# Kernel tuning notes

Hardware: AMD Instinct MI355X
Metric: run time of the kernel (lower is better)

Reference implementation:

```python
import jax, jax.numpy as jnp
import numpy as np

B, C, N = 32, 512, 1024   # batch, input channels, tokens
E, D, H = 512, 2048, 8    # d_input, d_model, heads
T, O = 50, 1000           # iterations, out_dims
NA, NO = 512, 512         # n_synch_action, n_synch_out


def setup_inputs() -> dict:
    key = jax.random.key(0)
    ks = jax.random.split(key, 16)
    s = 0.02
    rn = lambda k, shape: jax.random.normal(k, shape, jnp.float32) * s
    return dict(
        x=jax.random.normal(ks[0], (B, C, N), jnp.float32),
        W_kv=rn(ks[1], (C, E)), b_kv=jnp.zeros(E), g_kv=jnp.ones(E), be_kv=jnp.zeros(E),
        W_q=rn(ks[2], (NA, E)), b_q=jnp.zeros(E),
        W_in=rn(ks[3], (E, 3 * E)), b_in=jnp.zeros(3 * E),
        W_ao=rn(ks[4], (E, E)), b_ao=jnp.zeros(E),
        W_syn=rn(ks[5], (E + D, 2 * D)), b_syn=jnp.zeros(2 * D),
        g_syn=jnp.ones(D), be_syn=jnp.zeros(D),
        g_pm=jnp.ones(D), be_pm=jnp.zeros(D),
        W1=rn(ks[6], (D, D)), b1=jnp.zeros(D),
        W2=rn(ks[7], (D, D)), b2=jnp.zeros(D),
        start_state=jax.random.uniform(ks[8], (D,), jnp.float32, -0.1, 0.1),
        decay_action=jnp.zeros(NA), decay_out=jnp.zeros(NO),
        W_out=rn(ks[9], (NO, O)), b_out=jnp.zeros(O),
        idx_action=jax.random.permutation(ks[10], D)[:NA].astype(jnp.int32),
        idx_out=jax.random.permutation(ks[11], D)[:NO].astype(jnp.int32),
    )


def _ln(x, g, b, eps=1e-5):
    m = x.mean(-1, keepdims=True)
    v = ((x - m) ** 2).mean(-1, keepdims=True)
    return (x - m) * jax.lax.rsqrt(v + eps) * g + b


def reference(x, W_kv, b_kv, g_kv, be_kv, W_q, b_q, W_in, b_in, W_ao, b_ao,
              W_syn, b_syn, g_syn, be_syn, g_pm, be_pm, W1, b1, W2, b2,
              start_state, decay_action, decay_out, W_out, b_out,
              idx_action, idx_out):
    Bx = x.shape[0]
    hd = E // H
    # features: backbone='none', pos='none' -> flatten(2).transpose(1,2) then kv_proj
    feats = jnp.transpose(x, (0, 2, 1))                 # [B,N,C]
    kv = _ln(feats @ W_kv + b_kv, g_kv, be_kv)          # [B,N,E]
    # MHA K/V are constant across iterations -> hoist
    Wq_a, Wk_a, Wv_a = jnp.split(W_in, 3, axis=1)
    bq_a, bk_a, bv_a = jnp.split(b_in, 3)
    K = (kv @ Wk_a + bk_a).reshape(Bx, N, H, hd)
    V = (kv @ Wv_a + bv_a).reshape(Bx, N, H, hd)
    r_a = jnp.exp(-jnp.clip(decay_action, 0.0, 15.0))   # [NA]
    r_o = jnp.exp(-jnp.clip(decay_out, 0.0, 15.0))      # [NO]
    act0 = jnp.broadcast_to(start_state, (Bx, D))
    zA = jnp.zeros((Bx, NA), jnp.float32)
    zO = jnp.zeros((Bx, NO), jnp.float32)
    logO = jnp.log(jnp.float32(O))
    scale = 1.0 / jnp.sqrt(jnp.float32(hd))

    def step(carry, _):
        act, aA, bA, aO, bO = carry
        # action sync (left == right in the source, so products are squares)
        sel = act[:, idx_action]
        aA = r_a * aA + sel * sel
        bA = r_a * bA + 1.0
        syncA = aA * jax.lax.rsqrt(bA)                  # [B,NA]
        # cross-attention query
        q = syncA @ W_q + b_q                           # [B,E]
        qh = (q @ Wq_a + bq_a).reshape(Bx, H, hd)
        scores = jnp.einsum('bhd,bnhd->bhn', qh, K) * scale
        w = jax.nn.softmax(scores, axis=-1)
        attn = jnp.einsum('bhn,bnhd->bhd', w, V).reshape(Bx, E)
        attn = attn @ W_ao + b_ao
        # synapses: LazyLinear(2D) -> GLU -> LayerNorm (dropout=0)
        h = jnp.concatenate([attn, act], axis=-1) @ W_syn + b_syn
        a_half, g_half = jnp.split(h, 2, axis=-1)
        state = _ln(a_half * jax.nn.sigmoid(g_half), g_syn, be_syn)
        # post-synapse MLP: LN -> Linear -> ReLU -> Linear -> ReLU
        hpm = _ln(state, g_pm, be_pm)
        act = jax.nn.relu(jax.nn.relu(hpm @ W1 + b1) @ W2 + b2)
        # out sync
        selo = act[:, idx_out]
        aO = r_o * aO + selo * selo
        bO = r_o * bO + 1.0
        syncO = aO * jax.lax.rsqrt(bO)                  # [B,NO]
        pred = syncO @ W_out + b_out                    # [B,O]
        lp = jax.nn.log_softmax(pred, axis=-1)
        ne = -jnp.sum(jnp.exp(lp) * lp, axis=-1) / logO
        cert = jnp.stack([ne, 1.0 - ne], axis=-1)       # [B,2]
        return (act, aA, bA, aO, bO), (pred, cert, syncO)

    _, (preds, certs, syncs) = jax.lax.scan(step, (act0, zA, zA, zO, zO), None, length=T)
    predictions = jnp.transpose(preds, (1, 2, 0))       # [B,O,T]
    certainties = jnp.transpose(certs, (1, 2, 0))       # [B,2,T]
    return predictions, certainties, syncs[-1]
```

## Files before the change

kernel.cpp:

```cpp
#include <hip/hip_runtime.h>


typedef unsigned short u16;
typedef unsigned int uv4 __attribute__((ext_vector_type(4)));
typedef float fv4 __attribute__((ext_vector_type(4)));
typedef float fv2 __attribute__((ext_vector_type(2)));

__device__ __forceinline__ float bf2f(u16 u) {
    return __uint_as_float(((unsigned int)u) << 16);
}
__device__ __forceinline__ float bflo(unsigned int u) { return __uint_as_float(u << 16); }
__device__ __forceinline__ float bfhi(unsigned int u) { return __uint_as_float(u & 0xffff0000u); }
__device__ __forceinline__ u16 f2bf(float f) {
    unsigned int u = __float_as_uint(f);
    unsigned int r = u + 0x7fffu + ((u >> 16) & 1u);
    return (u16)(r >> 16);
}

__device__ __forceinline__ void cload(fv4& r, const void* p) {
    asm volatile("global_load_dwordx4 %0, %1, off sc0 sc1" : "=v"(r) : "v"(p));
}
__device__ __forceinline__ void cload2(fv2& r, const void* p) {
    asm volatile("global_load_dwordx2 %0, %1, off sc0 sc1" : "=v"(r) : "v"(p));
}
__device__ __forceinline__ void cstore4(void* p, fv4 v) {
    asm volatile("global_store_dwordx4 %0, %1, off sc0 sc1" :: "v"(p), "v"(v) : "memory");
}
__device__ __forceinline__ void cstore2(void* p, fv2 v) {
    asm volatile("global_store_dwordx2 %0, %1, off sc0 sc1" :: "v"(p), "v"(v) : "memory");
}
__device__ __forceinline__ void cwait1(fv4& a) {
    asm volatile("s_waitcnt vmcnt(0)" : "+v"(a) :: "memory");
    __builtin_amdgcn_sched_barrier(0);
}
__device__ __forceinline__ void cwait2(fv4& a, fv4& b) {
    asm volatile("s_waitcnt vmcnt(0)" : "+v"(a), "+v"(b) :: "memory");
    __builtin_amdgcn_sched_barrier(0);
}
__device__ __forceinline__ void cwait4(fv4& a, fv4& b, fv4& c, fv4& d) {
    asm volatile("s_waitcnt vmcnt(0)" : "+v"(a), "+v"(b), "+v"(c), "+v"(d) :: "memory");
    __builtin_amdgcn_sched_barrier(0);
}
__device__ __forceinline__ void cwait2x4(fv2& a, fv2& b, fv2& c, fv2& d) {
    asm volatile("s_waitcnt vmcnt(0)" : "+v"(a), "+v"(b), "+v"(c), "+v"(d) :: "memory");
    __builtin_amdgcn_sched_barrier(0);
}

__device__ __forceinline__ float aload(const float* p) {
    return __hip_atomic_load((const float*)p, __ATOMIC_RELAXED, __HIP_MEMORY_SCOPE_AGENT);
}

__global__ __launch_bounds__(256) void k_init(
    const float* __restrict__ start_state, const float* __restrict__ dec_a,
    const float* __restrict__ dec_o,
    float* act0, float* aA, float* bA, float* aO, float* bO,
    float* r_a, float* r_o, unsigned* bar)
{
    int g = blockIdx.x * 256 + threadIdx.x;
    int T = gridDim.x * 256;
    for (int i = g; i < 32 * 2048; i += T) act0[i] = start_state[i & 2047];
    for (int i = g; i < 32 * 512; i += T) { aA[i] = 0.f; bA[i] = 0.f; aO[i] = 0.f; bO[i] = 0.f; }
    for (int i = g; i < 512; i += T) {
        float da = fminf(fmaxf(dec_a[i], 0.f), 15.f);
        float dv = fminf(fmaxf(dec_o[i], 0.f), 15.f);
        r_a[i] = __expf(-da);
        r_o[i] = __expf(-dv);
    }
    if (g < 2048) bar[g] = 0u;
}

__global__ __launch_bounds__(256) void k_gemm_xT(
    const float* __restrict__ x, const float* __restrict__ Wkv,
    const float* __restrict__ bkv, float* __restrict__ out)
{
    __shared__ float As[16 * 68];
    __shared__ float Bs[16 * 132];
    int tid = threadIdx.x;
    int tn = tid & 15, tm = tid >> 4;
    int n0 = blockIdx.x * 128;
    int r0 = blockIdx.y * 64;
    int b = r0 >> 10;
    int nrow0 = r0 & 1023;
    const float* xb = x + (size_t)b * 512 * 1024;
    float acc[4][8];
#pragma unroll
    for (int i = 0; i < 4; ++i)
#pragma unroll
        for (int j = 0; j < 8; ++j) acc[i][j] = 0.f;

    for (int k0 = 0; k0 < 512; k0 += 16) {
        __syncthreads();
#pragma unroll
        for (int l = 0; l < 4; ++l) {
            int i = tid + l * 256;
            int nn = i & 63, kk = i >> 6;
            As[kk * 68 + nn] = xb[(size_t)(k0 + kk) * 1024 + nrow0 + nn];
        }
#pragma unroll
        for (int l = 0; l < 8; ++l) {
            int i = tid + l * 256;
            int n = i & 127, kk = i >> 7;
            Bs[kk * 132 + n] = Wkv[(size_t)(k0 + kk) * 512 + n0 + n];
        }
        __syncthreads();
#pragma unroll
        for (int k = 0; k < 16; ++k) {
            float4 a4 = *(const float4*)&As[k * 68 + tm * 4];
            float4 b0 = *(const float4*)&Bs[k * 132 + tn * 8];
            float4 b1 = *(const float4*)&Bs[k * 132 + tn * 8 + 4];
            float av[4] = {a4.x, a4.y, a4.z, a4.w};
            float bv[8] = {b0.x, b0.y, b0.z, b0.w, b1.x, b1.y, b1.z, b1.w};
#pragma unroll
            for (int i = 0; i < 4; ++i)
#pragma unroll
                for (int j = 0; j < 8; ++j) acc[i][j] += av[i] * bv[j];
        }
    }
#pragma unroll
    for (int i = 0; i < 4; ++i) {
        int r = r0 + tm * 4 + i;
        int c = n0 + tn * 8;
        float* orow = out + (size_t)r * 512 + c;
#pragma unroll
        for (int j = 0; j < 8; ++j) orow[j] = acc[i][j] + bkv[c + j];
    }
}

// ... 69 lines not shown
    float4 u1 = *(float4*)(p + 4);
    float v[8] = {u0.x, u0.y, u0.z, u0.w, u1.x, u1.y, u1.z, u1.w};
    float s = 0.f, s2 = 0.f;
#pragma unroll
    for (int i = 0; i < 8; ++i) { s += v[i]; s2 += v[i] * v[i]; }
#pragma unroll
    for (int off = 32; off >= 1; off >>= 1) {
        s += __shfl_xor(s, off, 64);
        s2 += __shfl_xor(s2, off, 64);
    }
    float m = s * (1.f / 512.f);
    float var = s2 * (1.f / 512.f) - m * m;
    float rs = rsqrtf(var + 1e-5f);
    const float* gp = g + lane * 8;
    const float* bp = be + lane * 8;
#pragma unroll
    for (int i = 0; i < 8; ++i) v[i] = (v[i] - m) * rs * gp[i] + bp[i];
    *(float4*)p = make_float4(v[0], v[1], v[2], v[3]);
    *(float4*)(p + 4) = make_float4(v[4], v[5], v[6], v[7]);
}

__global__ __launch_bounds__(256) void k_bvec(
    const float* __restrict__ vin, const float* __restrict__ B, int ldb,
    const float* __restrict__ badd, float* __restrict__ out, int Nj)
{
    int j = blockIdx.x * 256 + threadIdx.x;
    if (j >= Nj) return;
    float s = 0.f;
    for (int e = 0; e < 512; ++e) s += vin[e] * B[(size_t)e * ldb + j];
    out[j] = s + badd[j];
}

__global__ __launch_bounds__(256) void k_convert(
    const float* __restrict__ src, u16* __restrict__ dst, int n)
{
    int g = blockIdx.x * 256 + threadIdx.x;
    int T = gridDim.x * 256;
    for (int i = g; i < n; i += T) dst[i] = f2bf(src[i]);
}

__global__ __launch_bounds__(256) void k_transpose_wout(
    const float* __restrict__ W, u16* __restrict__ WT)
{
    int j = blockIdx.x * 256 + threadIdx.x;
    if (j >= 1000) return;
    for (int k = 0; k < 512; ++k) WT[(size_t)j * 512 + k] = f2bf(W[(size_t)k * 1000 + j]);
}

__global__ __launch_bounds__(256) void k_transpose_v(
    const u16* __restrict__ V, u16* __restrict__ VT)
{
    int bh = blockIdx.x;
    int b = bh >> 3, h = bh & 7;
    int tid = threadIdx.x;
    const u16* src = V + (size_t)b * 1024 * 512 + h * 64;
    u16* dst = VT + (size_t)bh * 64 * 1024;
    int n0 = tid * 4;
    for (int d = 0; d < 64; ++d) {
        u16 a0 = src[(size_t)(n0 + 0) * 512 + d];
        u16 a1 = src[(size_t)(n0 + 1) * 512 + d];
        u16 a2 = src[(size_t)(n0 + 2) * 512 + d];
        u16 a3 = src[(size_t)(n0 + 3) * 512 + d];
        uint2 w = make_uint2((unsigned)a0 | ((unsigned)a1 << 16),
                             (unsigned)a2 | ((unsigned)a3 << 16));
        *(uint2*)&dst[(size_t)d * 1024 + n0] = w;
    }
}

#define NBLK 1024

struct LoopP {
    const u16* Wqq; const float* bqq;
    const u16* K;   const u16* VT;
    const u16* Wfull; const float* bcomb;
    const u16* W1; const float* b1;
    const u16* W2; const float* b2;
    const u16* WoutT; const float* bout;
    const int* idxA; const int* idxO;
    const float* r_a; const float* r_o;
    float* aA0; float* aA1; float* bA0; float* bA1;
    float* aO0; float* aO1; float* bO0; float* bO1;
    float* act0; float* act1;
    float* pvp; float* mz;
    float* h_pre; float* hpm; float* t1;
    float* out;
    const float* gsyn; const float* besyn; const float* gpm; const float* bepm;
    unsigned* bar;
};

union Smem {
    struct { float sA[512]; float qh[64]; float sc[256]; float red[512]; } at;
    struct { float Al[32 * 36]; float wc[1024]; } sk;
    struct { float red[16]; } gl;
    struct { float sO[512]; float red[8]; } pr;
};

__device__ __forceinline__ void gridbar(unsigned* bar)
{
    __syncthreads();
    if (threadIdx.x == 0) {
        int blk = blockIdx.x;
        unsigned* cnt1 = bar + ((blk >> 6) << 5);
        unsigned* cnt2 = bar + (16 << 5);
        unsigned* genp = bar + ((17 + (blk & 31)) << 5);
        unsigned g = __hip_atomic_load(genp, __ATOMIC_RELAXED, __HIP_MEMORY_SCOPE_AGENT);
        asm volatile("s_waitcnt vmcnt(0)" ::: "memory");
        unsigned a = __hip_atomic_fetch_add(cnt1, 1u, __ATOMIC_RELAXED, __HIP_MEMORY_SCOPE_AGENT);
        if (a == 63u) {
            __hip_atomic_store(cnt1, 0u, __ATOMIC_RELAXED, __HIP_MEMORY_SCOPE_AGENT);
            asm volatile("s_waitcnt vmcnt(0)" ::: "memory");
            unsigned a2 = __hip_atomic_fetch_add(cnt2, 1u, __ATOMIC_RELAXED, __HIP_MEMORY_SCOPE_AGENT);
            if (a2 == 15u) {
                __hip_atomic_store(cnt2, 0u, __ATOMIC_RELAXED, __HIP_MEMORY_SCOPE_AGENT);
                asm volatile("s_waitcnt vmcnt(0)" ::: "memory");
#pragma unroll
                for (int r = 0; r < 32; ++r)
                    __hip_atomic_store(bar + ((17 + r) << 5), g + 1u,
                                       __ATOMIC_RELAXED, __HIP_MEMORY_SCOPE_AGENT);
            }
        }
        unsigned cur;
        do {
            cur = __hip_atomic_load(genp, __ATOMIC_RELAXED, __HIP_MEMORY_SCOPE_AGENT);
            if (cur != g) break;
            __builtin_amdgcn_s_sleep(2);
        } while (true);
        asm volatile("" ::: "memory");
    }
    __syncthreads();
}

__device__ __forceinline__ void red2(float& a, float& b, float* red, int tid)
{
#pragma unroll
    for (int off = 32; off >= 1; off >>= 1) {
        a += __shfl_xor(a, off, 64);
        b += __shfl_xor(b, off, 64);
    }
    __syncthreads();
    if ((tid & 63) == 0) { red[(tid >> 6) * 2] = a; red[(tid >> 6) * 2 + 1] = b; }
    __syncthreads();
    float sa = 0.f, sb = 0.f;
#pragma unroll
    for (int w = 0; w < 8; ++w) { sa += red[2 * w]; sb += red[2 * w + 1]; }
    a = sa; b = sb;
}

__global__ __launch_bounds__(512, 8) void k_loop(LoopP P)
{
    __shared__ Smem s;
    const int tid = threadIdx.x;
    const int blk = blockIdx.x;
    const int lane = tid & 63;
    const int wav = tid >> 6;

    for (int t = 0; t < 50; ++t) {
        const float* actprev = (t & 1) ? P.act1 : P.act0;
        float*       actnext = (t & 1) ? P.act0 : P.act1;
        const float* aAp = (t & 1) ? P.aA1 : P.aA0;  float* aAc = (t & 1) ? P.aA0 : P.aA1;
        const float* bAp = (t & 1) ? P.bA1 : P.bA0;  float* bAc = (t & 1) ? P.bA0 : P.bA1;
        const float* aOp = (t & 1) ? P.aO1 : P.aO0;  float* aOc = (t & 1) ? P.aO0 : P.aO1;
        const float* bOp = (t & 1) ? P.bO1 : P.bO0;  float* bOc = (t & 1) ? P.bO0 : P.bO1;

        __syncthreads();

        {
            int bh = blk >> 2, p = blk & 3;
            int b = bh >> 3, h = bh & 7;
            if (tid < 64) {
                int g4 = blk * 64 + tid;
                fv4 zz = {0.f, 0.f, 0.f, 0.f};
                if (g4 < 32768) cstore4(&P.h_pre[g4 * 4], zz);
                else if (g4 < 49152) cstore4(&P.t1[(g4 - 32768) * 4], zz);
                else cstore4(&actnext[(g4 - 49152) * 4], zz);
            }
            {
                int j = tid;
                int ia = P.idxA[j];
                float v = aload(&actprev[b * 2048 + ia]);
                if (t > 0) v = fmaxf(0.f, v + P.b2[ia]);
                float r = P.r_a[j];
                float a = r * aAp[b * 512 + j] + v * v;
                float bb = r * bAp[b * 512 + j] + 1.f;
                aAc[b * 512 + j] = a; bAc[b * 512 + j] = bb;
                s.at.sA[j] = a * rsqrtf(bb);
            }
            __syncthreads();
            {
                int d = tid & 63, kg = tid >> 6;
                const u16* wp = P.Wqq + (size_t)(kg * 64) * 512 + h * 64 + d;
                const float* ap = s.at.sA + kg * 64;
                float pq = 0.f;
#pragma unroll 16
                for (int k = 0; k < 64; ++k) pq += ap[k] * bf2f(wp[(size_t)k * 512]);
                s.at.red[tid] = pq;
            }
            __syncthreads();
            if (tid < 64) {
                float q = P.bqq[h * 64 + tid];
#pragma unroll
                for (int g2 = 0; g2 < 8; ++g2) q += s.at.red[g2 * 64 + tid];
                s.at.qh[tid] = q;
            }
            __syncthreads();
            if (tid < 256) {
                const u16* Kbh = P.K + (size_t)b * 1024 * 512 + h * 64;
                const uv4* kp = (const uv4*)(Kbh + (size_t)(p * 256 + tid) * 512);
                uv4 u[8];
#pragma unroll
                for (int i = 0; i < 8; ++i) u[i] = __builtin_nontemporal_load(kp + i);
                float dot = 0.f;
#pragma unroll
                for (int i = 0; i < 8; ++i) {
                    float4 q0 = *(float4*)&s.at.qh[i * 8];
                    float4 q1 = *(float4*)&s.at.qh[i * 8 + 4];
                    dot += q0.x * bflo(u[i].x) + q0.y * bfhi(u[i].x)
                         + q0.z * bflo(u[i].y) + q0.w * bfhi(u[i].y)
                         + q1.x * bflo(u[i].z) + q1.y * bfhi(u[i].z)
                         + q1.z * bflo(u[i].w) + q1.w * bfhi(u[i].w);
                }
                s.at.sc[tid] = dot * 0.125f;
            }
            __syncthreads();
            float mv = (tid < 256) ? s.at.sc[tid] : -1e30f;
#pragma unroll
            for (int off = 32; off >= 1; off >>= 1) mv = fmaxf(mv, __shfl_xor(mv, off, 64));
            if (lane == 0) s.at.red[wav] = mv;
            __syncthreads();
            float mloc = s.at.red[0];
#pragma unroll
            for (int w = 1; w < 8; ++w) mloc = fmaxf(mloc, s.at.red[w]);
            float ev = 0.f;
            if (tid < 256) {
                ev = __expf(s.at.sc[tid] - mloc);
                s.at.sc[tid] = ev;
            }
            float zv = ev;
#pragma unroll
            for (int off = 32; off >= 1; off >>= 1) zv += __shfl_xor(zv, off, 64);
            __syncthreads();
            if (lane == 0) s.at.red[wav] = zv;
            __syncthreads();
            float Zloc = 0.f;
#pragma unroll
            for (int w = 0; w < 8; ++w) Zloc += s.at.red[w];
            __syncthreads();
            {
                int d = tid & 63, ng = tid >> 6;
                const uv4* vp = (const uv4*)(P.VT
                    + ((size_t)bh * 64 + d) * 1024 + p * 256 + ng * 32);
                float acc = 0.f;
#pragma unroll
                for (int i = 0; i < 4; ++i) {
                    uv4 u = __builtin_nontemporal_load(vp + i);
                    const float* so = s.at.sc + ng * 32 + i * 8;
                    acc += so[0] * bflo(u.x) + so[1] * bfhi(u.x)
                         + so[2] * bflo(u.y) + so[3] * bfhi(u.y)
                         + so[4] * bflo(u.z) + so[5] * bfhi(u.z)
                         + so[6] * bflo(u.w) + so[7] * bfhi(u.w);
                }
                s.at.red[tid] = acc;
            }
            __syncthreads();
            if (tid < 64) {
                float a = 0.f;
#pragma unroll
                for (int g2 = 0; g2 < 8; ++g2) a += s.at.red[g2 * 64 + tid];
                s.at.qh[tid] = a;
            }
            __syncthreads();
            if (tid < 16) {
                fv4 v = *(fv4*)&s.at.qh[tid * 4];
                cstore4(&P.pvp[((size_t)p * 256 + bh) * 64 + tid * 4], v);
            }
            if (tid == 0) {
                fv2 v; v.x = mloc; v.y = Zloc;
                cstore2(&P.mz[(p * 256 + bh) * 2], v);
            }
        }
        gridbar(P.bar);

        {
            if (tid < 256) {
                int rh = tid;
                fv2 m0, m1, m2, m3;
                cload2(m0, &P.mz[(0 * 256 + rh) * 2]);
                cload2(m1, &P.mz[(1 * 256 + rh) * 2]);
                cload2(m2, &P.mz[(2 * 256 + rh) * 2]);
                cload2(m3, &P.mz[(3 * 256 + rh) * 2]);
                cwait2x4(m0, m1, m2, m3);
                float M = fmaxf(fmaxf(m0.x, m1.x), fmaxf(m2.x, m3.x));
                float e0 = __expf(m0.x - M), e1 = __expf(m1.x - M);
                float e2 = __expf(m2.x - M), e3 = __expf(m3.x - M);
                float Z = m0.y * e0 + m1.y * e1 + m2.y * e2 + m3.y * e3;
                float inv = 1.f / Z;
                s.sk.wc[rh * 4 + 0] = e0 * inv;
                s.sk.wc[rh * 4 + 1] = e1 * inv;
                s.sk.wc[rh * 4 + 2] = e2 * inv;
                s.sk.wc[rh * 4 + 3] = e3 * inv;
            }
            int kb = blk >> 6, jb = blk & 63;
            int j = jb * 64 + (tid & 63);
            int rg = tid >> 6;
            int kbeg = kb * 160;
            float a0 = 0.f, a1 = 0.f, a2 = 0.f, a3 = 0.f;
            for (int k0 = kbeg; k0 < kbeg + 160; k0 += 32) {
                __syncthreads();
                if (tid < 256) {
                    int k4 = (tid & 7) * 4, r = tid >> 3;
                    int kk = k0 + k4;
                    fv4 v;
                    if (kk < 512) {
                        int h = kk >> 6, d = kk & 63;
                        int rh = r * 8 + h;
                        fv4 v0, v1, v2, v3;
                        cload(v0, &P.pvp[((size_t)0 * 256 + rh) * 64 + d]);
                        cload(v1, &P.pvp[((size_t)1 * 256 + rh) * 64 + d]);
                        cload(v2, &P.pvp[((size_t)2 * 256 + rh) * 64 + d]);
                        cload(v3, &P.pvp[((size_t)3 * 256 + rh) * 64 + d]);
                        cwait4(v0, v1, v2, v3);
                        const float* w = &s.sk.wc[rh * 4];
                        v = v0 * w[0] + v1 * w[1] + v2 * w[2] + v3 * w[3];
                    } else {
                        cload(v, &actprev[r * 2048 + kk - 512]);
                        cwait1(v);
                        if (t > 0) {
                            float4 b4 = *(const float4*)&P.b2[kk - 512];
                            v.x = fmaxf(0.f, v.x + b4.x);
                            v.y = fmaxf(0.f, v.y + b4.y);
                            v.z = fmaxf(0.f, v.z + b4.z);
                            v.w = fmaxf(0.f, v.w + b4.w);
                        }
                    }
                    s.sk.Al[(k4 + 0) * 36 + r] = v.x;
                    s.sk.Al[(k4 + 1) * 36 + r] = v.y;
                    s.sk.Al[(k4 + 2) * 36 + r] = v.z;
                    s.sk.Al[(k4 + 3) * 36 + r] = v.w;
                }
                __syncthreads();
                const u16* wp = P.Wfull + (size_t)k0 * 4096 + j;
#pragma unroll 32
                for (int k = 0; k < 32; ++k) {
                    float w = bf2f(wp[(size_t)k * 4096]);
                    float4 a = *(const float4*)&s.sk.Al[k * 36 + rg * 4];
                    a0 += a.x * w; a1 += a.y * w; a2 += a.z * w; a3 += a.w * w;
                }
            }
            int r0 = rg * 4;
            atomicAdd(&P.h_pre[(size_t)(r0 + 0) * 4096 + j], a0);
            atomicAdd(&P.h_pre[(size_t)(r0 + 1) * 4096 + j], a1);
            atomicAdd(&P.h_pre[(size_t)(r0 + 2) * 4096 + j], a2);
            atomicAdd(&P.h_pre[(size_t)(r0 + 3) * 4096 + j], a3);
        }
        gridbar(P.bar);

        if (blk < 32) {
            const float* hr = P.h_pre + (size_t)blk * 4096;
            int i4 = tid * 4;
            fv4 av, gv;
            cload(av, hr + i4);
            cload(gv, hr + 2048 + i4);
            cwait2(av, gv);
            float4 bc1 = *(const float4*)&P.bcomb[i4];
            float4 bc2 = *(const float4*)&P.bcomb[2048 + i4];
            fv4 z;
            z.x = (av.x + bc1.x) / (1.f + __expf(-(gv.x + bc2.x)));
            z.y = (av.y + bc1.y) / (1.f + __expf(-(gv.y + bc2.y)));
            z.z = (av.z + bc1.z) / (1.f + __expf(-(gv.z + bc2.z)));
            z.w = (av.w + bc1.w) / (1.f + __expf(-(gv.w + bc2.w)));
            float sa = z.x + z.y + z.z + z.w;
            float sb = z.x * z.x + z.y * z.y + z.z * z.z + z.w * z.w;
            red2(sa, sb, s.gl.red, tid);
            float m1 = sa * (1.f / 2048.f);
            float v1 = sb * (1.f / 2048.f) - m1 * m1;
            float rs1 = rsqrtf(v1 + 1e-5f);
            float4 gs = *(const float4*)&P.gsyn[i4];
            float4 bs = *(const float4*)&P.besyn[i4];
            z.x = (z.x - m1) * rs1 * gs.x + bs.x;
            z.y = (z.y - m1) * rs1 * gs.y + bs.y;
            z.z = (z.z - m1) * rs1 * gs.z + bs.z;
            z.w = (z.w - m1) * rs1 * gs.w + bs.w;
            float ta = z.x + z.y + z.z + z.w;
            float tb = z.x * z.x + z.y * z.y + z.z * z.z + z.w * z.w;
            red2(ta, tb, s.gl.red, tid);
            float m2 = ta * (1.f / 2048.f);
            float v2 = tb * (1.f / 2048.f) - m2 * m2;
            float rs2 = rsqrtf(v2 + 1e-5f);
            float4 gp = *(const float4*)&P.gpm[i4];
            float4 bp = *(const float4*)&P.bepm[i4];
            fv4 o;
            o.x = (z.x - m2) * rs2 * gp.x + bp.x;
            o.y = (z.y - m2) * rs2 * gp.y + bp.y;
            o.z = (z.z - m2) * rs2 * gp.z + bp.z;
            o.w = (z.w - m2) * rs2 * gp.w + bp.w;
            cstore4(&P.hpm[(size_t)blk * 2048 + i4], o);
        }
        gridbar(P.bar);

        {
            int kb = blk >> 5, jb = blk & 31;
            int j = jb * 64 + (tid & 63);
            int rg = tid >> 6;
            int kbeg = kb * 64;
            float a0 = 0.f, a1 = 0.f, a2 = 0.f, a3 = 0.f;
            for (int k0 = kbeg; k0 < kbeg + 64; k0 += 32) {
                __syncthreads();
                if (tid < 256) {
                    int k4 = (tid & 7) * 4, r = tid >> 3;
                    fv4 v;
                    cload(v, &P.hpm[r * 2048 + k0 + k4]);
                    cwait1(v);
                    s.sk.Al[(k4 + 0) * 36 + r] = v.x;
                    s.sk.Al[(k4 + 1) * 36 + r] = v.y;
                    s.sk.Al[(k4 + 2) * 36 + r] = v.z;
                    s.sk.Al[(k4 + 3) * 36 + r] = v.w;
                }
                __syncthreads();
                const u16* wp = P.W1 + (size_t)k0 * 2048 + j;
#pragma unroll 32
                for (int k = 0; k < 32; ++k) {
                    float w = bf2f(wp[(size_t)k * 2048]);
                    float4 a = *(const float4*)&s.sk.Al[k * 36 + rg * 4];
                    a0 += a.x * w; a1 += a.y * w; a2 += a.z * w; a3 += a.w * w;
                }
            }
            int r0 = rg * 4;
            atomicAdd(&P.t1[(r0 + 0) * 2048 + j], a0);
            atomicAdd(&P.t1[(r0 + 1) * 2048 + j], a1);
            atomicAdd(&P.t1[(r0 + 2) * 2048 + j], a2);
            atomicAdd(&P.t1[(r0 + 3) * 2048 + j], a3);
        }
        gridbar(P.bar);

        {
            int kb = blk >> 5, jb = blk & 31;
            int j = jb * 64 + (tid & 63);
            int rg = tid >> 6;
            int kbeg = kb * 64;
            float a0 = 0.f, a1 = 0.f, a2 = 0.f, a3 = 0.f;
            for (int k0 = kbeg; k0 < kbeg + 64; k0 += 32) {
                __syncthreads();
                if (tid < 256) {
                    int k4 = (tid & 7) * 4, r = tid >> 3;
                    int kk = k0 + k4;
                    fv4 v;
                    cload(v, &P.t1[r * 2048 + kk]);
                    cwait1(v);
                    float4 b4 = *(const float4*)&P.b1[kk];
                    s.sk.Al[(k4 + 0) * 36 + r] = fmaxf(0.f, v.x + b4.x);
                    s.sk.Al[(k4 + 1) * 36 + r] = fmaxf(0.f, v.y + b4.y);
                    s.sk.Al[(k4 + 2) * 36 + r] = fmaxf(0.f, v.z + b4.z);
                    s.sk.Al[(k4 + 3) * 36 + r] = fmaxf(0.f, v.w + b4.w);
                }
                __syncthreads();
                const u16* wp = P.W2 + (size_t)k0 * 2048 + j;
#pragma unroll 32
                for (int k = 0; k < 32; ++k) {
                    float w = bf2f(wp[(size_t)k * 2048]);
                    float4 a = *(const float4*)&s.sk.Al[k * 36 + rg * 4];
                    a0 += a.x * w; a1 += a.y * w; a2 += a.z * w; a3 += a.w * w;
                }
            }
            int r0 = rg * 4;
            atomicAdd(&actnext[(r0 + 0) * 2048 + j], a0);
            atomicAdd(&actnext[(r0 + 1) * 2048 + j], a1);
            atomicAdd(&actnext[(r0 + 2) * 2048 + j], a2);
            atomicAdd(&actnext[(r0 + 3) * 2048 + j], a3);
        }
        gridbar(P.bar);

        if (blk < 32) {
            int b = blk;
            {
                int j2 = tid;
                int io = P.idxO[j2];
                float v = fmaxf(0.f, aload(&actnext[b * 2048 + io]) + P.b2[io]);
                float r = P.r_o[j2];
                float a = r * aOp[b * 512 + j2] + v * v;
                float bb = r * bOp[b * 512 + j2] + 1.f;
                aOc[b * 512 + j2] = a; bOc[b * 512 + j2] = bb;
                float sy = a * rsqrtf(bb);
                s.pr.sO[j2] = sy;
                if (t == 49) P.out[1603200 + b * 512 + j2] = sy;
            }
            __syncthreads();
            bool has1 = tid < 488;
            float p0, p1 = -1e30f;
            {
                const uint4* wp = (const uint4*)(P.WoutT + (size_t)tid * 512);
                float acc = 0.f;
#pragma unroll 16
                for (int i = 0; i < 64; ++i) {
                    uint4 u = wp[i];
                    const float* so = s.pr.sO + i * 8;
                    acc += so[0] * bflo(u.x) + so[1] * bfhi(u.x)
                         + so[2] * bflo(u.y) + so[3] * bfhi(u.y)
                         + so[4] * bflo(u.z) + so[5] * bfhi(u.z)
                         + so[6] * bflo(u.w) + so[7] * bfhi(u.w);
                }
                p0 = acc + P.bout[tid];
            }
            if (has1) {
                const uint4* wp = (const uint4*)(P.WoutT + (size_t)(tid + 512) * 512);
                float acc = 0.f;
#pragma unroll 16
                for (int i = 0; i < 64; ++i) {
                    uint4 u = wp[i];
                    const float* so = s.pr.sO + i * 8;
                    acc += so[0] * bflo(u.x) + so[1] * bfhi(u.x)
                         + so[2] * bflo(u.y) + so[3] * bfhi(u.y)
                         + so[4] * bflo(u.z) + so[5] * bfhi(u.z)
                         + so[6] * bflo(u.w) + so[7] * bfhi(u.w);
                }
                p1 = acc + P.bout[tid + 512];
            }
            float mx = fmaxf(p0, p1);
#pragma unroll
            for (int off = 32; off >= 1; off >>= 1) mx = fmaxf(mx, __shfl_xor(mx, off, 64));
            __syncthreads();
            if (lane == 0) s.pr.red[wav] = mx;
            __syncthreads();
            mx = s.pr.red[0];
#pragma unroll
            for (int w = 1; w < 8; ++w) mx = fmaxf(mx, s.pr.red[w]);
            float zs = __expf(p0 - mx) + (has1 ? __expf(p1 - mx) : 0.f);
#pragma unroll
            for (int off = 32; off >= 1; off >>= 1) zs += __shfl_xor(zs, off, 64);
            __syncthreads();
            if (lane == 0) s.pr.red[wav] = zs;
            __syncthreads();
            float Z = 0.f;
#pragma unroll
            for (int w = 0; w < 8; ++w) Z += s.pr.red[w];
            float logZ = __logf(Z);
            float lp0 = p0 - mx - logZ;
            float se = __expf(lp0) * lp0;
            if (has1) { float lp1 = p1 - mx - logZ; se += __expf(lp1) * lp1; }
#pragma unroll
            for (int off = 32; off >= 1; off >>= 1) se += __shfl_xor(se, off, 64);
            __syncthreads();
            if (lane == 0) s.pr.red[wav] = se;
            __syncthreads();
            float S = 0.f;
#pragma unroll
            for (int w = 0; w < 8; ++w) S += s.pr.red[w];
            float ne = -S / logf(1000.0f);
            P.out[(size_t)b * 50000 + (size_t)tid * 50 + t] = p0;
            if (has1) P.out[(size_t)b * 50000 + (size_t)(tid + 512) * 50 + t] = p1;
            if (tid == 0) {
                P.out[1600000 + b * 100 + t] = ne;
                P.out[1600000 + b * 100 + 50 + t] = 1.f - ne;
            }
        }
    }
}

extern "C" void kernel_launch(void* const* d_in, const int* in_sizes, int n_in,
                              void* d_out, int out_size, void* d_ws, size_t ws_size,
                              hipStream_t stream)
{
    const float* x      = (const float*)d_in[0];
    const float* W_kv   = (const float*)d_in[1];
    const float* b_kv   = (const float*)d_in[2];
    const float* g_kv   = (const float*)d_in[3];
    const float* be_kv  = (const float*)d_in[4];
    const float* W_q    = (const float*)d_in[5];
    const float* b_q    = (const float*)d_in[6];
    const float* W_in   = (const float*)d_in[7];
    const float* b_in   = (const float*)d_in[8];
    const float* W_ao   = (const float*)d_in[9];
    const float* b_ao   = (const float*)d_in[10];
    const float* W_syn  = (const float*)d_in[11];
    const float* b_syn  = (const float*)d_in[12];
    const float* g_syn  = (const float*)d_in[13];
    const float* be_syn = (const float*)d_in[14];
    const float* g_pm   = (const float*)d_in[15];
    const float* be_pm  = (const float*)d_in[16];
    const float* W1     = (const float*)d_in[17];
    const float* b1     = (const float*)d_in[18];
    const float* W2     = (const float*)d_in[19];
    const float* b2     = (const float*)d_in[20];
    const float* start_state  = (const float*)d_in[21];
    const float* decay_action = (const float*)d_in[22];
    const float* decay_out    = (const float*)d_in[23];
    const float* W_out  = (const float*)d_in[24];
    const float* b_out  = (const float*)d_in[25];
    const int* idx_action = (const int*)d_in[26];
    const int* idx_out    = (const int*)d_in[27];
    float* out = (float*)d_out;

    char* ws = (char*)d_ws;
    size_t off = 0;
    auto take = [&](size_t bytes) -> char* {
        char* p = ws + off;
        off += (bytes + 255) & ~(size_t)255;
        return p;
    };

    char* region0 = take(67108864);
    float* kv = (float*)region0;
    u16* W_full = (u16*)region0;
    u16* W1b    = (u16*)(region0 + 20971520);
    u16* W2b    = (u16*)(region0 + 29360128);
    u16* WoutT  = (u16*)(region0 + 37748736);
    u16* Wqqb   = (u16*)(region0 + 38772736);

    u16* K_bf = (u16*)take(33554432);
    u16* V_bf = (u16*)take(33554432);
    u16* V_T  = (u16*)take(33554432);
    float* b_qq   = (float*)take(2048);
    float* b_comb = (float*)take(16384);
    float* r_a = (float*)take(2048);
    float* r_o = (float*)take(2048);
    float* aA0 = (float*)take(65536);
    float* aA1 = (float*)take(65536);
    float* bA0 = (float*)take(65536);
    float* bA1 = (float*)take(65536);
    float* aO0 = (float*)take(65536);
    float* aO1 = (float*)take(65536);
    float* bO0 = (float*)take(65536);
    float* bO1 = (float*)take(65536);
    float* act0v = (float*)take(262144);
    float* act1v = (float*)take(262144);
    float* h_pre = (float*)take(524288);
    float* hpm   = (float*)take(262144);
    float* t1_pre = (float*)take(262144);
    float* pvp = (float*)take(262144);
    float* mzB = (float*)take(8192);
    unsigned* bar = (unsigned*)take(8192);
    (void)ws_size; (void)in_sizes; (void)n_in; (void)out_size;

    k_init<<<256, 256, 0, stream>>>(start_state, decay_action, decay_out,
                                    act0v, aA0, bA0, aO0, bO0, r_a, r_o, bar);
    k_gemm_xT<<<dim3(4, 512), 256, 0, stream>>>(x, W_kv, b_kv, kv);
    k_ln_kv<<<8192, 256, 0, stream>>>(kv, g_kv, be_kv);
    k_gemm_AB<<<dim3(4, 512), 256, 0, stream>>>(kv, 512, W_in + 512, 1536, b_in + 512, K_bf, 512);
    k_gemm_AB<<<dim3(4, 512), 256, 0, stream>>>(kv, 512, W_in + 1024, 1536, b_in + 1024, V_bf, 512);
    k_transpose_v<<<256, 256, 0, stream>>>(V_bf, V_T);
    k_gemm_AB<<<dim3(4, 8), 256, 0, stream>>>(W_q, 512, W_in, 1536, nullptr, Wqqb, 512);
    k_gemm_AB<<<dim3(32, 8), 256, 0, stream>>>(W_ao, 512, W_syn, 4096, nullptr, W_full, 4096);
    k_bvec<<<2, 256, 0, stream>>>(b_q, W_in, 1536, b_in, b_qq, 512);
    k_bvec<<<16, 256, 0, stream>>>(b_ao, W_syn, 4096, b_syn, b_comb, 4096);
    k_convert<<<2048, 256, 0, stream>>>(W_syn + (size_t)512 * 4096, W_full + (size_t)512 * 4096, 2048 * 4096);
    k_convert<<<2048, 256, 0, stream>>>(W1, W1b, 2048 * 2048);
    k_convert<<<2048, 256, 0, stream>>>(W2, W2b, 2048 * 2048);
    k_transpose_wout<<<4, 256, 0, stream>>>(W_out, WoutT);

    LoopP p;
    p.Wqq = Wqqb; p.bqq = b_qq;
    p.K = K_bf;   p.VT = V_T;
    p.Wfull = W_full; p.bcomb = b_comb;
    p.W1 = W1b; p.b1 = b1;
    p.W2 = W2b; p.b2 = b2;
    p.WoutT = WoutT; p.bout = b_out;
    p.idxA = idx_action; p.idxO = idx_out;
    p.r_a = r_a; p.r_o = r_o;
    p.aA0 = aA0; p.aA1 = aA1; p.bA0 = bA0; p.bA1 = bA1;
    p.aO0 = aO0; p.aO1 = aO1; p.bO0 = bO0; p.bO1 = bO1;
    p.act0 = act0v; p.act1 = act1v;
    p.pvp = pvp; p.mz = mzB;
    p.h_pre = h_pre; p.hpm = hpm; p.t1 = t1_pre;
    p.out = out;
    p.gsyn = g_syn; p.besyn = be_syn; p.gpm = g_pm; p.bepm = be_pm;
    p.bar = bar;

    k_loop<<<dim3(NBLK), dim3(512), 0, stream>>>(p);
}
```

Before: 10.34 ms.

## Partition persistent-loop GEMVs by batch row instead of split-K with atomics

Reworks the three per-iteration matrix products (synapse, W1, W2) so each block owns one batch row and a column chunk, reducing over K inside the block through shared memory and writing results with plain stores. This removes the atomicAdd accumulation and the per-iteration zeroing of h_pre, t1 and act. The softmax-combined attention row and the relu'd previous activation are now precomputed into new buffers, which costs an extra grid barrier and phase. In exchange each block rereads its weight columns once per batch row, so total weight traffic from L2 rises by the batch factor compared with the old row-tiled reuse.

```diff
diff --git a/kernel.cpp b/kernel.cpp
--- a/kernel.cpp
+++ b/kernel.cpp
@@ -37,12 +37,8 @@
     asm volatile("s_waitcnt vmcnt(0)" : "+v"(a), "+v"(b) :: "memory");
     __builtin_amdgcn_sched_barrier(0);
 }
-__device__ __forceinline__ void cwait4(fv4& a, fv4& b, fv4& c, fv4& d) {
-    asm volatile("s_waitcnt vmcnt(0)" : "+v"(a), "+v"(b), "+v"(c), "+v"(d) :: "memory");
-    __builtin_amdgcn_sched_barrier(0);
-}
-__device__ __forceinline__ void cwait2x4(fv2& a, fv2& b, fv2& c, fv2& d) {
-    asm volatile("s_waitcnt vmcnt(0)" : "+v"(a), "+v"(b), "+v"(c), "+v"(d) :: "memory");
+__device__ __forceinline__ void cwaitf2(fv2& a) {
+    asm volatile("s_waitcnt vmcnt(0)" : "+v"(a) :: "memory");
     __builtin_amdgcn_sched_barrier(0);
 }
 
@@ -278,6 +274,7 @@
     float* aO0; float* aO1; float* bO0; float* bO1;
     float* act0; float* act1;
     float* pvp; float* mz;
+    float* attn_f; float* actR;
     float* h_pre; float* hpm; float* t1;
     float* out;
     const float* gsyn; const float* besyn; const float* gpm; const float* bepm;
@@ -286,7 +283,9 @@
 
 union Smem {
     struct { float sA[512]; float qh[64]; float sc[256]; float red[512]; } at;
-    struct { float Al[32 * 36]; float wc[1024]; } sk;
+    struct { float mzs[64]; float arow[512]; } b2;
+    struct { float As[2560]; float red[512]; float orow[128]; } ck;
+    struct { float As[2048]; float red[512]; float orow[64]; } ek;
     struct { float red[16]; } gl;
     struct { float sO[512]; float red[8]; } pr;
 };
@@ -363,12 +362,19 @@
         {
             int bh = blk >> 2, p = blk & 3;
             int b = bh >> 3, h = bh & 7;
-            if (tid < 64) {
-                int g4 = blk * 64 + tid;
-                fv4 zz = {0.f, 0.f, 0.f, 0.f};
-                if (g4 < 32768) cstore4(&P.h_pre[g4 * 4], zz);
-                else if (g4 < 49152) cstore4(&P.t1[(g4 - 32768) * 4], zz);
-                else cstore4(&actnext[(g4 - 49152) * 4], zz);
+            if (p == 0 && tid < 64) {
+                int i4 = (h * 64 + tid) * 4;
+                fv4 v;
+                cload(v, &actprev[b * 2048 + i4]);
+                cwait1(v);
+                if (t > 0) {
+                    float4 b4 = *(const float4*)&P.b2[i4];
+                    v.x = fmaxf(0.f, v.x + b4.x);
+                    v.y = fmaxf(0.f, v.y + b4.y);
+                    v.z = fmaxf(0.f, v.z + b4.z);
+                    v.w = fmaxf(0.f, v.w + b4.w);
+                }
+                cstore4(&P.actR[b * 2048 + i4], v);
             }
             {
                 int j = tid;
@@ -476,77 +482,73 @@
         }
         gridbar(P.bar);
 
+        if (blk < 32) {
+            int b = blk;
+            if (tid < 32) {
+                int p = tid >> 3, h = tid & 7;
+                fv2 v;
+                cload2(v, &P.mz[(p * 256 + b * 8 + h) * 2]);
+                cwaitf2(v);
+                s.b2.mzs[tid * 2] = v.x;
+                s.b2.mzs[tid * 2 + 1] = v.y;
+            }
+            __syncthreads();
+            int h = tid >> 6, d = tid & 63;
+            int rh = b * 8 + h;
+            float m0 = s.b2.mzs[(0 * 8 + h) * 2], z0 = s.b2.mzs[(0 * 8 + h) * 2 + 1];
+            float m1 = s.b2.mzs[(1 * 8 + h) * 2], z1 = s.b2.mzs[(1 * 8 + h) * 2 + 1];
+            float m2 = s.b2.mzs[(2 * 8 + h) * 2], z2 = s.b2.mzs[(2 * 8 + h) * 2 + 1];
+            float m3 = s.b2.mzs[(3 * 8 + h) * 2], z3 = s.b2.mzs[(3 * 8 + h) * 2 + 1];
+            float M = fmaxf(fmaxf(m0, m1), fmaxf(m2, m3));
+            float e0 = __expf(m0 - M), e1 = __expf(m1 - M);
+            float e2 = __expf(m2 - M), e3 = __expf(m3 - M);
+            float Zinv = 1.f / (z0 * e0 + z1 * e1 + z2 * e2 + z3 * e3);
+            float acc = aload(&P.pvp[((size_t)0 * 256 + rh) * 64 + d]) * e0
+                      + aload(&P.pvp[((size_t)1 * 256 + rh) * 64 + d]) * e1
+                      + aload(&P.pvp[((size_t)2 * 256 + rh) * 64 + d]) * e2
+                      + aload(&P.pvp[((size_t)3 * 256 + rh) * 64 + d]) * e3;
+            s.b2.arow[tid] = acc * Zinv;
+            __syncthreads();
+            if (tid < 128) {
+                fv4 v = *(fv4*)&s.b2.arow[tid * 4];
+                cstore4(&P.attn_f[b * 512 + tid * 4], v);
+            }
+        }
+        gridbar(P.bar);
+
         {
-            if (tid < 256) {
-                int rh = tid;
-                fv2 m0, m1, m2, m3;
-                cload2(m0, &P.mz[(0 * 256 + rh) * 2]);
-                cload2(m1, &P.mz[(1 * 256 + rh) * 2]);
-                cload2(m2, &P.mz[(2 * 256 + rh) * 2]);
-                cload2(m3, &P.mz[(3 * 256 + rh) * 2]);
-                cwait2x4(m0, m1, m2, m3);
-                float M = fmaxf(fmaxf(m0.x, m1.x), fmaxf(m2.x, m3.x));
-                float e0 = __expf(m0.x - M), e1 = __expf(m1.x - M);
-                float e2 = __expf(m2.x - M), e3 = __expf(m3.x - M);
-                float Z = m0.y * e0 + m1.y * e1 + m2.y * e2 + m3.y * e3;
-                float inv = 1.f / Z;
-                s.sk.wc[rh * 4 + 0] = e0 * inv;
-                s.sk.wc[rh * 4 + 1] = e1 * inv;
-                s.sk.wc[rh * 4 + 2] = e2 * inv;
-                s.sk.wc[rh * 4 + 3] = e3 * inv;
-            }
-            int kb = blk >> 6, jb = blk & 63;
-            int j = jb * 64 + (tid & 63);
-            int rg = tid >> 6;
-            int kbeg = kb * 160;
-            float a0 = 0.f, a1 = 0.f, a2 = 0.f, a3 = 0.f;
-            for (int k0 = kbeg; k0 < kbeg + 160; k0 += 32) {
-                __syncthreads();
-                if (tid < 256) {
-                    int k4 = (tid & 7) * 4, r = tid >> 3;
-                    int kk = k0 + k4;
-                    fv4 v;
-                    if (kk < 512) {
-                        int h = kk >> 6, d = kk & 63;
-                        int rh = r * 8 + h;
-                        fv4 v0, v1, v2, v3;
-                        cload(v0, &P.pvp[((size_t)0 * 256 + rh) * 64 + d]);
-                        cload(v1, &P.pvp[((size_t)1 * 256 + rh) * 64 + d]);
-                        cload(v2, &P.pvp[((size_t)2 * 256 + rh) * 64 + d]);
-                        cload(v3, &P.pvp[((size_t)3 * 256 + rh) * 64 + d]);
-                        cwait4(v0, v1, v2, v3);
-                        const float* w = &s.sk.wc[rh * 4];
-                        v = v0 * w[0] + v1 * w[1] + v2 * w[2] + v3 * w[3];
-                    } else {
-                        cload(v, &actprev[r * 2048 + kk - 512]);
-                        cwait1(v);
-                        if (t > 0) {
-                            float4 b4 = *(const float4*)&P.b2[kk - 512];
-                            v.x = fmaxf(0.f, v.x + b4.x);
-                            v.y = fmaxf(0.f, v.y + b4.y);
-                            v.z = fmaxf(0.f, v.z + b4.z);
-                            v.w = fmaxf(0.f, v.w + b4.w);
-                        }
-                    }
-                    s.sk.Al[(k4 + 0) * 36 + r] = v.x;
-                    s.sk.Al[(k4 + 1) * 36 + r] = v.y;
-                    s.sk.Al[(k4 + 2) * 36 + r] = v.z;
-                    s.sk.Al[(k4 + 3) * 36 + r] = v.w;
-                }
-                __syncthreads();
-                const u16* wp = P.Wfull + (size_t)k0 * 4096 + j;
+            int b = blk >> 5, jc = blk & 31;
+            int j0 = jc * 128;
+            if (tid < 128) {
+                fv4 v; cload(v, &P.attn_f[b * 512 + tid * 4]); cwait1(v);
+                *(fv4*)&s.ck.As[tid * 4] = v;
+            } else {
+                fv4 v; cload(v, &P.actR[b * 2048 + (tid - 128) * 4]); cwait1(v);
+                *(fv4*)&s.ck.As[512 + (tid - 128) * 4] = v;
+            }
+            if (tid < 128) {
+                fv4 v; cload(v, &P.actR[b * 2048 + (384 + tid) * 4]); cwait1(v);
+                *(fv4*)&s.ck.As[512 + (384 + tid) * 4] = v;
+            }
+            __syncthreads();
+            int j = j0 + (tid & 127);
+            int kq = tid >> 7;
+            const u16* wp = P.Wfull + (size_t)(kq * 640) * 4096 + j;
+            const float* ap = s.ck.As + kq * 640;
+            float acc = 0.f;
 #pragma unroll 32
-                for (int k = 0; k < 32; ++k) {
-                    float w = bf2f(wp[(size_t)k * 4096]);
-                    float4 a = *(const float4*)&s.sk.Al[k * 36 + rg * 4];
-                    a0 += a.x * w; a1 += a.y * w; a2 += a.z * w; a3 += a.w * w;
-                }
-            }
-            int r0 = rg * 4;
-            atomicAdd(&P.h_pre[(size_t)(r0 + 0) * 4096 + j], a0);
-            atomicAdd(&P.h_pre[(size_t)(r0 + 1) * 4096 + j], a1);
-            atomicAdd(&P.h_pre[(size_t)(r0 + 2) * 4096 + j], a2);
-            atomicAdd(&P.h_pre[(size_t)(r0 + 3) * 4096 + j], a3);
+            for (int k = 0; k < 640; ++k) acc += ap[k] * bf2f(wp[(size_t)k * 4096]);
+            s.ck.red[kq * 128 + (tid & 127)] = acc;
+            __syncthreads();
+            if (tid < 128) {
+                s.ck.orow[tid] = s.ck.red[tid] + s.ck.red[128 + tid]
+                               + s.ck.red[256 + tid] + s.ck.red[384 + tid];
+            }
+            __syncthreads();
+            if (tid < 32) {
+                fv4 v = *(fv4*)&s.ck.orow[tid * 4];
+                cstore4(&P.h_pre[(size_t)b * 4096 + j0 + tid * 4], v);
+            }
         }
         gridbar(P.bar);
 
@@ -594,74 +596,67 @@
         gridbar(P.bar);
 
         {
-            int kb = blk >> 5, jb = blk & 31;
-            int j = jb * 64 + (tid & 63);
-            int rg = tid >> 6;
-            int kbeg = kb * 64;
-            float a0 = 0.f, a1 = 0.f, a2 = 0.f, a3 = 0.f;
-            for (int k0 = kbeg; k0 < kbeg + 64; k0 += 32) {
-                __syncthreads();
-                if (tid < 256) {
-                    int k4 = (tid & 7) * 4, r = tid >> 3;
-                    fv4 v;
-                    cload(v, &P.hpm[r * 2048 + k0 + k4]);
-                    cwait1(v);
-                    s.sk.Al[(k4 + 0) * 36 + r] = v.x;
-                    s.sk.Al[(k4 + 1) * 36 + r] = v.y;
-                    s.sk.Al[(k4 + 2) * 36 + r] = v.z;
-                    s.sk.Al[(k4 + 3) * 36 + r] = v.w;
-                }
-                __syncthreads();
-                const u16* wp = P.W1 + (size_t)k0 * 2048 + j;
+            int b = blk >> 5, jc = blk & 31;
+            int j0 = jc * 64;
+            {
+                fv4 v; cload(v, &P.hpm[(size_t)b * 2048 + tid * 4]); cwait1(v);
+                *(fv4*)&s.ek.As[tid * 4] = v;
+            }
+            __syncthreads();
+            int j = j0 + (tid & 63), kq = tid >> 6;
+            const u16* wp = P.W1 + (size_t)(kq * 256) * 2048 + j;
+            const float* ap = s.ek.As + kq * 256;
+            float acc = 0.f;
 #pragma unroll 32
-                for (int k = 0; k < 32; ++k) {
-                    float w = bf2f(wp[(size_t)k * 2048]);
-                    float4 a = *(const float4*)&s.sk.Al[k * 36 + rg * 4];
-                    a0 += a.x * w; a1 += a.y * w; a2 += a.z * w; a3 += a.w * w;
-                }
-            }
-            int r0 = rg * 4;
-            atomicAdd(&P.t1[(r0 + 0) * 2048 + j], a0);
-            atomicAdd(&P.t1[(r0 + 1) * 2048 + j], a1);
-            atomicAdd(&P.t1[(r0 + 2) * 2048 + j], a2);
-            atomicAdd(&P.t1[(r0 + 3) * 2048 + j], a3);
+            for (int k = 0; k < 256; ++k) acc += ap[k] * bf2f(wp[(size_t)k * 2048]);
+            s.ek.red[kq * 64 + (tid & 63)] = acc;
+            __syncthreads();
+            if (tid < 64) {
+                float v = 0.f;
+#pragma unroll
+                for (int q = 0; q < 8; ++q) v += s.ek.red[q * 64 + tid];
+                s.ek.orow[tid] = v;
+            }
+            __syncthreads();
+            if (tid < 16) {
+                fv4 v = *(fv4*)&s.ek.orow[tid * 4];
+                cstore4(&P.t1[(size_t)b * 2048 + j0 + tid * 4], v);
+            }
         }
         gridbar(P.bar);
 
         {
-            int kb = blk >> 5, jb = blk & 31;
-            int j = jb * 64 + (tid & 63);
-            int rg = tid >> 6;
-            int kbeg = kb * 64;
-            float a0 = 0.f, a1 = 0.f, a2 = 0.f, a3 = 0.f;
-            for (int k0 = kbeg; k0 < kbeg + 64; k0 += 32) {
-                __syncthreads();
-                if (tid < 256) {
-                    int k4 = (tid & 7) * 4, r = tid >> 3;
-                    int kk = k0 + k4;
-                    fv4 v;
-                    cload(v, &P.t1[r * 2048 + kk]);
-                    cwait1(v);
-                    float4 b4 = *(const float4*)&P.b1[kk];
-                    s.sk.Al[(k4 + 0) * 36 + r] = fmaxf(0.f, v.x + b4.x);
-                    s.sk.Al[(k4 + 1) * 36 + r] = fmaxf(0.f, v.y + b4.y);
-                    s.sk.Al[(k4 + 2) * 36 + r] = fmaxf(0.f, v.z + b4.z);
-                    s.sk.Al[(k4 + 3) * 36 + r] = fmaxf(0.f, v.w + b4.w);
-                }
-                __syncthreads();
-                const u16* wp = P.W2 + (size_t)k0 * 2048 + j;
+            int b = blk >> 5, jc = blk & 31;
+            int j0 = jc * 64;
+            {
+                fv4 v; cload(v, &P.t1[(size_t)b * 2048 + tid * 4]); cwait1(v);
+                float4 b4 = *(const float4*)&P.b1[tid * 4];
+                v.x = fmaxf(0.f, v.x + b4.x);
+                v.y = fmaxf(0.f, v.y + b4.y);
+                v.z = fmaxf(0.f, v.z + b4.z);
+                v.w = fmaxf(0.f, v.w + b4.w);
+                *(fv4*)&s.ek.As[tid * 4] = v;
+            }
+            __syncthreads();
+            int j = j0 + (tid & 63), kq = tid >> 6;
+            const u16* wp = P.W2 + (size_t)(kq * 256) * 2048 + j;
+            const float* ap = s.ek.As + kq * 256;
+            float acc = 0.f;
 #pragma unroll 32
-                for (int k = 0; k < 32; ++k) {
-                    float w = bf2f(wp[(size_t)k * 2048]);
-                    float4 a = *(const float4*)&s.sk.Al[k * 36 + rg * 4];
-                    a0 += a.x * w; a1 += a.y * w; a2 += a.z * w; a3 += a.w * w;
-                }
-            }
-            int r0 = rg * 4;
-            atomicAdd(&actnext[(r0 + 0) * 2048 + j], a0);
-            atomicAdd(&actnext[(r0 + 1) * 2048 + j], a1);
-            atomicAdd(&actnext[(r0 + 2) * 2048 + j], a2);
-            atomicAdd(&actnext[(r0 + 3) * 2048 + j], a3);
+            for (int k = 0; k < 256; ++k) acc += ap[k] * bf2f(wp[(size_t)k * 2048]);
+            s.ek.red[kq * 64 + (tid & 63)] = acc;
+            __syncthreads();
+            if (tid < 64) {
+                float v = 0.f;
+#pragma unroll
+                for (int q = 0; q < 8; ++q) v += s.ek.red[q * 64 + tid];
+                s.ek.orow[tid] = v;
+            }
+            __syncthreads();
+            if (tid < 16) {
+                fv4 v = *(fv4*)&s.ek.orow[tid * 4];
+                cstore4(&actnext[(size_t)b * 2048 + j0 + tid * 4], v);
+            }
         }
         gridbar(P.bar);
 
@@ -823,6 +818,8 @@
     float* t1_pre = (float*)take(262144);
     float* pvp = (float*)take(262144);
     float* mzB = (float*)take(8192);
+    float* attn_f = (float*)take(65536);
+    float* actR   = (float*)take(262144);
     unsigned* bar = (unsigned*)take(8192);
     (void)ws_size; (void)in_sizes; (void)n_in; (void)out_size;
 
@@ -855,6 +852,7 @@
     p.aO0 = aO0; p.aO1 = aO1; p.bO0 = bO0; p.bO1 = bO1;
     p.act0 = act0v; p.act1 = act1v;
     p.pvp = pvp; p.mz = mzB;
+    p.attn_f = attn_f; p.actR = actR;
     p.h_pre = h_pre; p.hpm = hpm; p.t1 = t1_pre;
     p.out = out;
     p.gsyn = g_syn; p.besyn = be_syn; p.gpm = g_pm; p.bepm = be_pm;
```

New measurement: 19.56 ms. 1.89x slower.

## Precombine split-softmax attention once per batch row before synapse GEMM

Applied to the files above, without the earlier changes.

The split-K attention partials (four partitions of m/Z and PV) are now merged once per batch row by 32 blocks into a compact attn_f buffer, behind an extra grid barrier. Previously every synapse GEMM block redid this merge while staging its A tile. The bias+ReLU on the previous activation is likewise done once in the attention phase and written to actR. This removes redundant global loads and arithmetic from the GEMM staging, at the cost of an extra grid-wide barrier each iteration and some extra global traffic.

```diff
diff --git a/kernel.cpp b/kernel.cpp
--- a/kernel.cpp
+++ b/kernel.cpp
@@ -37,12 +37,8 @@
     asm volatile("s_waitcnt vmcnt(0)" : "+v"(a), "+v"(b) :: "memory");
     __builtin_amdgcn_sched_barrier(0);
 }
-__device__ __forceinline__ void cwait4(fv4& a, fv4& b, fv4& c, fv4& d) {
-    asm volatile("s_waitcnt vmcnt(0)" : "+v"(a), "+v"(b), "+v"(c), "+v"(d) :: "memory");
-    __builtin_amdgcn_sched_barrier(0);
-}
-__device__ __forceinline__ void cwait2x4(fv2& a, fv2& b, fv2& c, fv2& d) {
-    asm volatile("s_waitcnt vmcnt(0)" : "+v"(a), "+v"(b), "+v"(c), "+v"(d) :: "memory");
+__device__ __forceinline__ void cwaitf2(fv2& a) {
+    asm volatile("s_waitcnt vmcnt(0)" : "+v"(a) :: "memory");
     __builtin_amdgcn_sched_barrier(0);
 }
 
@@ -278,6 +274,7 @@
     float* aO0; float* aO1; float* bO0; float* bO1;
     float* act0; float* act1;
     float* pvp; float* mz;
+    float* attn_f; float* actR;
     float* h_pre; float* hpm; float* t1;
     float* out;
     const float* gsyn; const float* besyn; const float* gpm; const float* bepm;
@@ -286,7 +283,8 @@
 
 union Smem {
     struct { float sA[512]; float qh[64]; float sc[256]; float red[512]; } at;
-    struct { float Al[32 * 36]; float wc[1024]; } sk;
+    struct { float mzs[64]; float arow[512]; } b2;
+    struct { float Al[32 * 36]; } sk;
     struct { float red[16]; } gl;
     struct { float sO[512]; float red[8]; } pr;
 };
@@ -370,6 +368,20 @@
                 else if (g4 < 49152) cstore4(&P.t1[(g4 - 32768) * 4], zz);
                 else cstore4(&actnext[(g4 - 49152) * 4], zz);
             }
+            if (p == 0 && tid >= 64 && tid < 128) {
+                int i4 = (h * 64 + (tid - 64)) * 4;
+                fv4 v;
+                cload(v, &actprev[b * 2048 + i4]);
+                cwait1(v);
+                if (t > 0) {
+                    float4 b4 = *(const float4*)&P.b2[i4];
+                    v.x = fmaxf(0.f, v.x + b4.x);
+                    v.y = fmaxf(0.f, v.y + b4.y);
+                    v.z = fmaxf(0.f, v.z + b4.z);
+                    v.w = fmaxf(0.f, v.w + b4.w);
+                }
+                cstore4(&P.actR[b * 2048 + i4], v);
+            }
             {
                 int j = tid;
                 int ia = P.idxA[j];
@@ -476,25 +488,41 @@
         }
         gridbar(P.bar);
 
+        if (blk < 32) {
+            int b = blk;
+            if (tid < 32) {
+                int p = tid >> 3, h = tid & 7;
+                fv2 v;
+                cload2(v, &P.mz[(p * 256 + b * 8 + h) * 2]);
+                cwaitf2(v);
+                s.b2.mzs[tid * 2] = v.x;
+                s.b2.mzs[tid * 2 + 1] = v.y;
+            }
+            __syncthreads();
+            int h = tid >> 6, d = tid & 63;
+            int rh = b * 8 + h;
+            float m0 = s.b2.mzs[(0 * 8 + h) * 2], z0 = s.b2.mzs[(0 * 8 + h) * 2 + 1];
+            float m1 = s.b2.mzs[(1 * 8 + h) * 2], z1 = s.b2.mzs[(1 * 8 + h) * 2 + 1];
+            float m2 = s.b2.mzs[(2 * 8 + h) * 2], z2 = s.b2.mzs[(2 * 8 + h) * 2 + 1];
+            float m3 = s.b2.mzs[(3 * 8 + h) * 2], z3 = s.b2.mzs[(3 * 8 + h) * 2 + 1];
+            float M = fmaxf(fmaxf(m0, m1), fmaxf(m2, m3));
+            float e0 = __expf(m0 - M), e1 = __expf(m1 - M);
+            float e2 = __expf(m2 - M), e3 = __expf(m3 - M);
+            float Zinv = 1.f / (z0 * e0 + z1 * e1 + z2 * e2 + z3 * e3);
+            float acc = aload(&P.pvp[((size_t)0 * 256 + rh) * 64 + d]) * e0
+                      + aload(&P.pvp[((size_t)1 * 256 + rh) * 64 + d]) * e1
+                      + aload(&P.pvp[((size_t)2 * 256 + rh) * 64 + d]) * e2
+                      + aload(&P.pvp[((size_t)3 * 256 + rh) * 64 + d]) * e3;
+            s.b2.arow[tid] = acc * Zinv;
+            __syncthreads();
+            if (tid < 128) {
+                fv4 v = *(fv4*)&s.b2.arow[tid * 4];
+                cstore4(&P.attn_f[b * 512 + tid * 4], v);
+            }
+        }
+        gridbar(P.bar);
+
         {
-            if (tid < 256) {
-                int rh = tid;
-                fv2 m0, m1, m2, m3;
-                cload2(m0, &P.mz[(0 * 256 + rh) * 2]);
-                cload2(m1, &P.mz[(1 * 256 + rh) * 2]);
-                cload2(m2, &P.mz[(2 * 256 + rh) * 2]);
-                cload2(m3, &P.mz[(3 * 256 + rh) * 2]);
-                cwait2x4(m0, m1, m2, m3);
-                float M = fmaxf(fmaxf(m0.x, m1.x), fmaxf(m2.x, m3.x));
-                float e0 = __expf(m0.x - M), e1 = __expf(m1.x - M);
-                float e2 = __expf(m2.x - M), e3 = __expf(m3.x - M);
-                float Z = m0.y * e0 + m1.y * e1 + m2.y * e2 + m3.y * e3;
-                float inv = 1.f / Z;
-                s.sk.wc[rh * 4 + 0] = e0 * inv;
-                s.sk.wc[rh * 4 + 1] = e1 * inv;
-                s.sk.wc[rh * 4 + 2] = e2 * inv;
-                s.sk.wc[rh * 4 + 3] = e3 * inv;
-            }
             int kb = blk >> 6, jb = blk & 63;
             int j = jb * 64 + (tid & 63);
             int rg = tid >> 6;
@@ -507,26 +535,11 @@
                     int kk = k0 + k4;
                     fv4 v;
                     if (kk < 512) {
-                        int h = kk >> 6, d = kk & 63;
-                        int rh = r * 8 + h;
-                        fv4 v0, v1, v2, v3;
-                        cload(v0, &P.pvp[((size_t)0 * 256 + rh) * 64 + d]);
-                        cload(v1, &P.pvp[((size_t)1 * 256 + rh) * 64 + d]);
-                        cload(v2, &P.pvp[((size_t)2 * 256 + rh) * 64 + d]);
-                        cload(v3, &P.pvp[((size_t)3 * 256 + rh) * 64 + d]);
-                        cwait4(v0, v1, v2, v3);
-                        const float* w = &s.sk.wc[rh * 4];
-                        v = v0 * w[0] + v1 * w[1] + v2 * w[2] + v3 * w[3];
+                        cload(v, &P.attn_f[r * 512 + kk]);
+                        cwait1(v);
                     } else {
-                        cload(v, &actprev[r * 2048 + kk - 512]);
+                        cload(v, &P.actR[r * 2048 + kk - 512]);
                         cwait1(v);
-                        if (t > 0) {
-                            float4 b4 = *(const float4*)&P.b2[kk - 512];
-                            v.x = fmaxf(0.f, v.x + b4.x);
-                            v.y = fmaxf(0.f, v.y + b4.y);
-                            v.z = fmaxf(0.f, v.z + b4.z);
-                            v.w = fmaxf(0.f, v.w + b4.w);
-                        }
                     }
                     s.sk.Al[(k4 + 0) * 36 + r] = v.x;
                     s.sk.Al[(k4 + 1) * 36 + r] = v.y;
@@ -823,6 +836,8 @@
     float* t1_pre = (float*)take(262144);
     float* pvp = (float*)take(262144);
     float* mzB = (float*)take(8192);
+    float* attn_f = (float*)take(65536);
+    float* actR   = (float*)take(262144);
     unsigned* bar = (unsigned*)take(8192);
     (void)ws_size; (void)in_sizes; (void)n_in; (void)out_size;
 
@@ -855,6 +870,7 @@
     p.aO0 = aO0; p.aO1 = aO1; p.bO0 = bO0; p.bO1 = bO1;
     p.act0 = act0v; p.act1 = act1v;
     p.pvp = pvp; p.mz = mzB;
+    p.attn_f = attn_f; p.actR = actR;
     p.h_pre = h_pre; p.hpm = hpm; p.t1 = t1_pre;
     p.out = out;
     p.gsyn = g_syn; p.besyn = be_syn; p.gpm = g_pm; p.bepm = be_pm;
```

Measured after the change: 10.32 ms. Within noise of the previous version (-0.1%).
